# Performance work log

Measured on AMD Instinct MI355X. Metric: run time of the kernel, lower is better.

## Reference

```python
import jax, jax.numpy as jnp
import numpy as np

FEATS, HID, LAT = 128, 64, 16
T = 131072


def _prelu(x, a):
    return jnp.where(x > 0, x, a * x)


def setup_inputs() -> dict:
    key = jax.random.key(0)
    ks = jax.random.split(key, 24)
    s = 0.05
    inp = {
        "x": jax.random.normal(ks[0], (T, FEATS), jnp.float32),
        "eps": jax.random.normal(ks[1], (T, LAT), jnp.float32),
        "h0": jax.random.uniform(ks[2], (HID,), jnp.float32),
        "c0": jax.random.normal(ks[3], (HID,), jnp.float32),
        "training": 1,
        # LSTM (torch gate order i,f,g,o)
        "W_ih": jax.random.normal(ks[4], (4 * HID, FEATS), jnp.float32) * s,
        "W_hh": jax.random.normal(ks[5], (4 * HID, HID), jnp.float32) * s,
        "b_ih": jax.random.normal(ks[6], (4 * HID,), jnp.float32) * s,
        "b_hh": jax.random.normal(ks[7], (4 * HID,), jnp.float32) * s,
        # encoder: Linear(H,H) PReLU Linear(H,H) PReLU Linear(H,2L)
        "We1": jax.random.normal(ks[8], (HID, HID), jnp.float32) * s,
        "be1": jax.random.normal(ks[9], (HID,), jnp.float32) * s,
        "ae1": jnp.array(0.25, jnp.float32),
        "We2": jax.random.normal(ks[10], (HID, HID), jnp.float32) * s,
        "be2": jax.random.normal(ks[11], (HID,), jnp.float32) * s,
        "ae2": jnp.array(0.25, jnp.float32),
        "We3": jax.random.normal(ks[12], (2 * LAT, HID), jnp.float32) * s,
        "be3": jax.random.normal(ks[13], (2 * LAT,), jnp.float32) * s,
        # decoder: Linear(L,H) PReLU Linear(H,H) PReLU Linear(H,F) Tanh
        "Wd1": jax.random.normal(ks[14], (HID, LAT), jnp.float32) * s,
        "bd1": jax.random.normal(ks[15], (HID,), jnp.float32) * s,
        "ad1": jnp.array(0.25, jnp.float32),
        "Wd2": jax.random.normal(ks[16], (HID, HID), jnp.float32) * s,
        "bd2": jax.random.normal(ks[17], (HID,), jnp.float32) * s,
        "ad2": jnp.array(0.25, jnp.float32),
        "Wd3": jax.random.normal(ks[18], (FEATS, HID), jnp.float32) * s,
        "bd3": jax.random.normal(ks[19], (FEATS,), jnp.float32) * s,
    }
    return inp


def reference(x, eps, h0, c0, training, W_ih, W_hh, b_ih, b_hh,
              We1, be1, ae1, We2, be2, ae2, We3, be3,
              Wd1, bd1, ad1, Wd2, bd2, ad2, Wd3, bd3):
    b = b_ih + b_hh

    def step(carry, xs):
        h, c = carry
        xt, et = xs
        gates = xt @ W_ih.T + h @ W_hh.T + b          # [4H]
        i, f, g, o = jnp.split(gates, 4)
        i, f, o = jax.nn.sigmoid(i), jax.nn.sigmoid(f), jax.nn.sigmoid(o)
        c2 = f * c + i * jnp.tanh(g)
        h2 = o * jnp.tanh(c2)
        e = _prelu(h2 @ We1.T + be1, ae1)
        e = _prelu(e @ We2.T + be2, ae2)
        ml = e @ We3.T + be3                          # [2L]
        mu, lv = ml[:LAT], ml[LAT:]
        z = mu + et * jnp.exp(0.5 * lv) if training else mu
        d = _prelu(z @ Wd1.T + bd1, ad1)
        d = _prelu(d @ Wd2.T + bd2, ad2)
        out = 4.0 * jnp.tanh(d @ Wd3.T + bd3)         # [F]
        return (h2, c2), (out, mu, lv)

    (_, _), (outs, mus, lvs) = jax.lax.scan(step, (h0, c0), (x, eps))
    return outs, mus, lvs
```

## Files before the change

### kernel.cpp

```cpp
#include <hip/hip_runtime.h>
#include <cstdint>

#define T_STEPS 131072
#define FEATS 128
#define HID 64
#define LAT 16
#define GATES 256

typedef float v4f __attribute__((ext_vector_type(4)));

#define LOG2E 1.44269504088896340736f

__device__ __forceinline__ float frcp(float x) { return __builtin_amdgcn_rcpf(x); }
__device__ __forceinline__ float fexp2(float x) { return __builtin_amdgcn_exp2f(x); }

__device__ __forceinline__ float tanh_f(float x) {
  float ax = fabsf(x);
  float e = fexp2(ax * (-2.0f * LOG2E));
  float r = (1.0f - e) * frcp(1.0f + e);
  return copysignf(r, x);
}
__device__ __forceinline__ float prelu(float x, float a) { return x > 0.0f ? x : a * x; }

__global__ __launch_bounds__(256) void kA(const float* __restrict__ x,
                                          const float* __restrict__ W_ih,
                                          const float* __restrict__ b_ih,
                                          const float* __restrict__ b_hh,
                                          float* __restrict__ xg,
                                          int t0, int n) {
  __shared__ float wt[FEATS * 128];
  __shared__ __align__(16) float xb[4][FEATS];
  const int tid = threadIdx.x;
  const int w = tid >> 6, l = tid & 63;
  const int half = blockIdx.x & 1;
  const int pair = blockIdx.x >> 1;

  for (int idx = tid; idx < 128 * FEATS; idx += 256) {
    int jj = idx >> 7, k = idx & 127;
    wt[k * 128 + jj] = W_ih[(size_t)(half * 128 + jj) * FEATS + k];
  }
  const int j0 = half * 128 + 2 * l;
  const float b0 = b_ih[j0] + b_hh[j0];
  const float b1 = b_ih[j0 + 1] + b_hh[j0 + 1];
  __syncthreads();

  for (int s = pair * 4 + w; s < n; s += 1024) {
    const size_t t = (size_t)(t0 + s);
    *(float2*)&xb[w][2 * l] = *(const float2*)&x[t * FEATS + 2 * l];
    float a0 = b0, a0b = 0.f, a1 = b1, a1b = 0.f;
#pragma unroll
    for (int k = 0; k < FEATS; k += 4) {
      float4 xk = *(const float4*)&xb[w][k];
      float2 w0 = *(const float2*)&wt[(k + 0) * 128 + 2 * l];
      float2 w1 = *(const float2*)&wt[(k + 1) * 128 + 2 * l];
      float2 w2 = *(const float2*)&wt[(k + 2) * 128 + 2 * l];
      float2 w3 = *(const float2*)&wt[(k + 3) * 128 + 2 * l];
      a0  += xk.x * w0.x; a0b += xk.y * w1.x;
      a0  += xk.z * w2.x; a0b += xk.w * w3.x;
      a1  += xk.x * w0.y; a1b += xk.y * w1.y;
      a1  += xk.z * w2.y; a1b += xk.w * w3.y;
    }
    *(float2*)&xg[(size_t)s * GATES + j0] = make_float2(a0 + a0b, a1 + a1b);
  }
}

#define BAR() asm volatile("s_waitcnt lgkmcnt(0)\ns_barrier" ::: "memory")

__global__ __launch_bounds__(256, 1) void kB(const float* __restrict__ xg,
                                             const float* __restrict__ W_hh,
                                             const float* __restrict__ h0,
                                             const float* __restrict__ c0,
                                             float* __restrict__ state,
                                             float* __restrict__ h2out,
                                             int t0, int nsteps, int first) {
  __shared__ __align__(16) float hbuf[2][HID];
  const int tid = threadIdx.x;
  const int w = tid >> 6;
  const int lane = tid & 63;
  const int le = lane & 15;
  const int g = lane >> 4;
  const int e = (w << 4) | le;
  const int j = (g << 6) | e;
  const bool isg2 = (g == 2);
  const float kmul2 = isg2 ? (-2.0f * LOG2E) : (-LOG2E);
  const int adr_f = (16 + le) << 2;
  const int adr_g = (32 + le) << 2;
  const int adr_o = (48 + le) << 2;

  v4f wreg[16];
#pragma unroll
  for (int k = 0; k < 16; ++k) wreg[k] = *(const v4f*)&W_hh[(size_t)j * HID + 4 * k];

  if (tid < HID) hbuf[0][tid] = first ? h0[tid] : state[tid];
  float c_reg = (lane < 16) ? (first ? c0[e] : state[HID + e]) : 0.0f;

  float x0 = xg[(size_t)0 * GATES + j];
  float x1 = xg[(size_t)1 * GATES + j];
  float x2 = xg[(size_t)2 * GATES + j];
  float x3 = xg[(size_t)3 * GATES + j];
  __syncthreads();

#define LSTM_STEP(XV, S, CUR)                                              \
  {                                                                        \
    const v4f* hb4 = (const v4f*)hbuf[CUR];                                \
    v4f ac0 = {(XV), 0.f, 0.f, 0.f};                                       \
    v4f ac1 = {0.f, 0.f, 0.f, 0.f};                                        \
    v4f ac2 = {0.f, 0.f, 0.f, 0.f};                                        \
    v4f ac3 = {0.f, 0.f, 0.f, 0.f};                                        \
    _Pragma("unroll")                                                      \
    for (int kk = 0; kk < 16; kk += 4) {                                   \
      ac0 = __builtin_elementwise_fma(hb4[kk + 0], wreg[kk + 0], ac0);     \
      ac1 = __builtin_elementwise_fma(hb4[kk + 1], wreg[kk + 1], ac1);     \
      ac2 = __builtin_elementwise_fma(hb4[kk + 2], wreg[kk + 2], ac2);     \
      ac3 = __builtin_elementwise_fma(hb4[kk + 3], wreg[kk + 3], ac3);     \
    }                                                                      \
    v4f av = (ac0 + ac1) + (ac2 + ac3);                                    \
    float acc = (av.x + av.y) + (av.z + av.w);                             \
    float ax = fabsf(acc);                                                 \
    float e_ = fexp2(kmul2 * ax);                                          \
    float rn = frcp(1.0f + e_);                                            \
    float pos = isg2 ? (1.0f - e_) * rn : rn;                              \
    float neg = isg2 ? -pos : e_ * rn;                                     \
    float a = (acc >= 0.0f) ? pos : neg;                                   \
    int ai = __float_as_int(a);                                            \
    float fv = __int_as_float(__builtin_amdgcn_ds_bpermute(adr_f, ai));    \
    float gv = __int_as_float(__builtin_amdgcn_ds_bpermute(adr_g, ai));    \
    float ov = __int_as_float(__builtin_amdgcn_ds_bpermute(adr_o, ai));    \
    float c2 = fv * c_reg + a * gv;                                        \
    float h2v = ov * tanh_f(c2);                                           \
    c_reg = c2;                                                            \
    if (lane < 16) {                                                       \
      hbuf[(CUR) ^ 1][e] = h2v;                                            \
      h2out[(size_t)(t0 + (S)) * 128 + e] = h2v;                           \
    }                                                                      \
    BAR();                                                                 \
  }

  for (int s = 0; s < nsteps; s += 4) {
    { float nx = xg[(size_t)(s + 4) * GATES + j]; LSTM_STEP(x0, s + 0, 0); x0 = nx; }
    { float nx = xg[(size_t)(s + 5) * GATES + j]; LSTM_STEP(x1, s + 1, 1); x1 = nx; }
    { float nx = xg[(size_t)(s + 6) * GATES + j]; LSTM_STEP(x2, s + 2, 0); x2 = nx; }
    { float nx = xg[(size_t)(s + 7) * GATES + j]; LSTM_STEP(x3, s + 3, 1); x3 = nx; }
  }
  if (tid < HID) state[tid] = hbuf[0][tid];
  if (lane < 16) state[HID + e] = c_reg;
#undef LSTM_STEP
}

__device__ __forceinline__ void stageT(float* dst, const float* __restrict__ src,
                                       int rows, int colsShift, int tid, int nthr) {
  const int total = rows << colsShift;
  const int cmask = (1 << colsShift) - 1;
  for (int idx = tid; idx < total; idx += nthr) {
    int jr = idx >> colsShift, k = idx & cmask;
    dst[k * rows + jr] = src[idx];
  }
}

__global__ __launch_bounds__(512) void kC(const float* __restrict__ eps,
                                          const int* __restrict__ trainp,
                                          const float* __restrict__ We1, const float* __restrict__ be1, const float* __restrict__ ae1,
                                          const float* __restrict__ We2, const float* __restrict__ be2, const float* __restrict__ ae2,
                                          const float* __restrict__ We3, const float* __restrict__ be3,
                                          const float* __restrict__ Wd1, const float* __restrict__ bd1, const float* __restrict__ ad1,
                                          const float* __restrict__ Wd2, const float* __restrict__ bd2, const float* __restrict__ ad2,
                                          const float* __restrict__ Wd3, const float* __restrict__ bd3,
                                          float* __restrict__ out) {
  __shared__ float wt1[4096], wt2[4096], wt3[2048], wtd1[1024], wtd2[4096], wtd3[8192];
  __shared__ float bb[416];
  __shared__ __align__(16) float abuf[8][2][HID];
  const int tid = threadIdx.x;

  stageT(wt1, We1, 64, 6, tid, 512);
  stageT(wt2, We2, 64, 6, tid, 512);
  stageT(wt3, We3, 32, 6, tid, 512);
  stageT(wtd1, Wd1, 64, 4, tid, 512);
  stageT(wtd2, Wd2, 64, 6, tid, 512);
  stageT(wtd3, Wd3, 128, 6, tid, 512);
  for (int i = tid; i < 416; i += 512) {
    float v;
    if (i < 64)       v = be1[i];
    else if (i < 128) v = be2[i - 64];
    else if (i < 160) v = be3[i - 128];
    else if (i < 224) v = bd1[i - 160];
    else if (i < 288) v = bd2[i - 224];
    else              v = bd3[i - 288];
    bb[i] = v;
  }
  const float a1 = *ae1, a2 = *ae2, ad1v = *ad1, ad2v = *ad2;
  const int train = *trainp;
  __syncthreads();

  const int w = tid >> 6, l = tid & 63, le = l & 15;
  float* bufA = abuf[w][0];
  float* bufB = abuf[w][1];

  for (int it = 0; it < 64; ++it) {
    const size_t t = ((size_t)blockIdx.x << 9) + (size_t)(it << 3) + (size_t)w;
    bufA[l] = out[t * 128 + l];
    {
      float accA = bb[l], accB = 0.f;
#pragma unroll
      for (int k = 0; k < 64; k += 4) {
        float4 v = *(const float4*)&bufA[k];
        accA += v.x * wt1[(k + 0) * 64 + l];
        accB += v.y * wt1[(k + 1) * 64 + l];
        accA += v.z * wt1[(k + 2) * 64 + l];
        accB += v.w * wt1[(k + 3) * 64 + l];
      }
      bufB[l] = prelu(accA + accB, a1);
    }
    {
      float accA = bb[64 + l], accB = 0.f;
#pragma unroll
      for (int k = 0; k < 64; k += 4) {
        float4 v = *(const float4*)&bufB[k];
        accA += v.x * wt2[(k + 0) * 64 + l];
        accB += v.y * wt2[(k + 1) * 64 + l];
        accA += v.z * wt2[(k + 2) * 64 + l];
        accB += v.w * wt2[(k + 3) * 64 + l];
      }
      bufA[l] = prelu(accA + accB, a2);
    }
    float m;
    {
      const int jj = l & 31;
      float accA = bb[128 + jj], accB = 0.f;
#pragma unroll
      for (int k = 0; k < 64; k += 4) {
        float4 v = *(const float4*)&bufA[k];
        accA += v.x * wt3[(k + 0) * 32 + jj];
        accB += v.y * wt3[(k + 1) * 32 + jj];
        accA += v.z * wt3[(k + 2) * 32 + jj];
        accB += v.w * wt3[(k + 3) * 32 + jj];
      }
      m = accA + accB;
    }
    if (l < 16)      out[(size_t)T_STEPS * 128 + t * LAT + l] = m;
    else if (l < 32) out[(size_t)T_STEPS * 144 + t * LAT + (l - 16)] = m;
    float muv = __shfl(m, le);
    float lvv = __shfl(m, 16 + le);
    float ev = eps[t * LAT + le];
    float z = train ? (muv + ev * fexp2(0.5f * LOG2E * lvv)) : muv;
    if (l < 16) bufB[l] = z;
    {
      float accA = bb[160 + l], accB = 0.f;
#pragma unroll
      for (int k = 0; k < 16; k += 4) {
        float4 v = *(const float4*)&bufB[k];
        accA += v.x * wtd1[(k + 0) * 64 + l];
        accB += v.y * wtd1[(k + 1) * 64 + l];
        accA += v.z * wtd1[(k + 2) * 64 + l];
        accB += v.w * wtd1[(k + 3) * 64 + l];
      }
      bufA[l] = prelu(accA + accB, ad1v);
    }
    {
      float accA = bb[224 + l], accB = 0.f;
#pragma unroll
      for (int k = 0; k < 64; k += 4) {
        float4 v = *(const float4*)&bufA[k];
        accA += v.x * wtd2[(k + 0) * 64 + l];
        accB += v.y * wtd2[(k + 1) * 64 + l];
        accA += v.z * wtd2[(k + 2) * 64 + l];
        accB += v.w * wtd2[(k + 3) * 64 + l];
      }
      bufB[l] = prelu(accA + accB, ad2v);
    }
    {
      float acc0 = bb[288 + 2 * l], acc0b = 0.f;
      float acc1 = bb[288 + 2 * l + 1], acc1b = 0.f;
#pragma unroll
      for (int k = 0; k < 64; k += 2) {
        float2 v = *(const float2*)&bufB[k];
        float2 w0 = *(const float2*)&wtd3[(k + 0) * 128 + 2 * l];
        float2 w1 = *(const float2*)&wtd3[(k + 1) * 128 + 2 * l];
        acc0  += v.x * w0.x; acc0b += v.y * w1.x;
        acc1  += v.x * w0.y; acc1b += v.y * w1.y;
      }
      float o0 = 4.0f * tanh_f(acc0 + acc0b);
      float o1 = 4.0f * tanh_f(acc1 + acc1b);
      *(float2*)&out[t * 128 + 2 * l] = make_float2(o0, o1);
    }
  }
}

extern "C" void kernel_launch(void* const* d_in, const int* in_sizes, int n_in,
                              void* d_out, int out_size, void* d_ws, size_t ws_size,
                              hipStream_t stream) {
  (void)in_sizes; (void)n_in; (void)out_size;
  const float* x    = (const float*)d_in[0];
  const float* eps  = (const float*)d_in[1];
  const float* h0   = (const float*)d_in[2];
  const float* c0   = (const float*)d_in[3];
  const int*   tr   = (const int*)d_in[4];
  const float* W_ih = (const float*)d_in[5];
  const float* W_hh = (const float*)d_in[6];
  const float* b_ih = (const float*)d_in[7];
  const float* b_hh = (const float*)d_in[8];
  const float* We1  = (const float*)d_in[9];
  const float* be1  = (const float*)d_in[10];
  const float* ae1  = (const float*)d_in[11];
  const float* We2  = (const float*)d_in[12];
  const float* be2  = (const float*)d_in[13];
  const float* ae2  = (const float*)d_in[14];
  const float* We3  = (const float*)d_in[15];
  const float* be3  = (const float*)d_in[16];
  const float* Wd1  = (const float*)d_in[17];
  const float* bd1  = (const float*)d_in[18];
  const float* ad1  = (const float*)d_in[19];
  const float* Wd2  = (const float*)d_in[20];
  const float* bd2  = (const float*)d_in[21];
  const float* ad2  = (const float*)d_in[22];
  const float* Wd3  = (const float*)d_in[23];
  const float* bd3  = (const float*)d_in[24];
  float* out = (float*)d_out;

  char* ws = (char*)d_ws;
  float* state = (float*)ws;
  float* xg    = (float*)(ws + 1024);

  long fit = (ws_size > 2048) ? (long)((ws_size - 1024) / (GATES * sizeof(float))) - 8 : 0;
  long ch = (fit < (long)T_STEPS) ? fit : (long)T_STEPS;
  ch &= ~3L;
  if (ch < 1024) ch = 1024;

  for (long t0 = 0; t0 < T_STEPS; t0 += ch) {
    int n = (int)(((long)T_STEPS - t0 < ch) ? ((long)T_STEPS - t0) : ch);
    hipLaunchKernelGGL(kA, dim3(512), dim3(256), 0, stream,
                       x, W_ih, b_ih, b_hh, xg, (int)t0, n);
    hipLaunchKernelGGL(kB, dim3(1), dim3(256), 0, stream,
                       xg, W_hh, h0, c0, state, out, (int)t0, n, (t0 == 0) ? 1 : 0);
  }
  hipLaunchKernelGGL(kC, dim3(256), dim3(512), 0, stream,
                     eps, tr, We1, be1, ae1, We2, be2, ae2, We3, be3,
                     Wd1, bd1, ad1, Wd2, bd2, ad2, Wd3, bd3, out);
}
```

Measured before the change: 55.03 ms.

## Run LSTM recurrence in a single wavefront with per-unit gate ownership

Result: slower. 131.4 ms (+138.7%).

```diff
diff --git a/kernel.cpp b/kernel.cpp
--- a/kernel.cpp
+++ b/kernel.cpp
@@ -14,9 +14,13 @@
 __device__ __forceinline__ float frcp(float x) { return __builtin_amdgcn_rcpf(x); }
 __device__ __forceinline__ float fexp2(float x) { return __builtin_amdgcn_exp2f(x); }
 
+__device__ __forceinline__ float sigm_f(float x) {
+  float e = fexp2(-LOG2E * fabsf(x));
+  float r = frcp(1.0f + e);
+  return x >= 0.0f ? r : e * r;
+}
 __device__ __forceinline__ float tanh_f(float x) {
-  float ax = fabsf(x);
-  float e = fexp2(ax * (-2.0f * LOG2E));
+  float e = fexp2(-2.0f * LOG2E * fabsf(x));
   float r = (1.0f - e) * frcp(1.0f + e);
   return copysignf(r, x);
 }
@@ -42,6 +46,8 @@
   const int j0 = half * 128 + 2 * l;
   const float b0 = b_ih[j0] + b_hh[j0];
   const float b1 = b_ih[j0 + 1] + b_hh[j0 + 1];
+  const int g0 = j0 >> 6;
+  const int e0 = j0 & 63;
   __syncthreads();
 
   for (int s = pair * 4 + w; s < n; s += 1024) {
@@ -60,90 +66,79 @@
       a1  += xk.x * w0.y; a1b += xk.y * w1.y;
       a1  += xk.z * w2.y; a1b += xk.w * w3.y;
     }
-    *(float2*)&xg[(size_t)s * GATES + j0] = make_float2(a0 + a0b, a1 + a1b);
-  }
-}
-
-#define BAR() asm volatile("s_waitcnt lgkmcnt(0)\ns_barrier" ::: "memory")
-
-__global__ __launch_bounds__(256, 1) void kB(const float* __restrict__ xg,
-                                             const float* __restrict__ W_hh,
-                                             const float* __restrict__ h0,
-                                             const float* __restrict__ c0,
-                                             float* __restrict__ state,
-                                             float* __restrict__ h2out,
-                                             int t0, int nsteps, int first) {
-  __shared__ __align__(16) float hbuf[2][HID];
-  const int tid = threadIdx.x;
-  const int w = tid >> 6;
-  const int lane = tid & 63;
-  const int le = lane & 15;
-  const int g = lane >> 4;
-  const int e = (w << 4) | le;
-  const int j = (g << 6) | e;
-  const bool isg2 = (g == 2);
-  const float kmul2 = isg2 ? (-2.0f * LOG2E) : (-LOG2E);
-  const int adr_f = (16 + le) << 2;
-  const int adr_g = (32 + le) << 2;
-  const int adr_o = (48 + le) << 2;
-
-  v4f wreg[16];
-#pragma unroll
-  for (int k = 0; k < 16; ++k) wreg[k] = *(const v4f*)&W_hh[(size_t)j * HID + 4 * k];
-
-  if (tid < HID) hbuf[0][tid] = first ? h0[tid] : state[tid];
-  float c_reg = (lane < 16) ? (first ? c0[e] : state[HID + e]) : 0.0f;
-
-  float x0 = xg[(size_t)0 * GATES + j];
-  float x1 = xg[(size_t)1 * GATES + j];
-  float x2 = xg[(size_t)2 * GATES + j];
-  float x3 = xg[(size_t)3 * GATES + j];
-  __syncthreads();
-
-#define LSTM_STEP(XV, S, CUR)                                              \
+    float* dst = &xg[(size_t)s * GATES];
+    dst[e0 * 4 + g0]       = a0 + a0b;
+    dst[(e0 + 1) * 4 + g0] = a1 + a1b;
+  }
+}
+
+__global__ __launch_bounds__(64, 1) void kB(const float4* __restrict__ xg4,
+                                            const float* __restrict__ W_hh,
+                                            const float* __restrict__ h0,
+                                            const float* __restrict__ c0,
+                                            float* __restrict__ state,
+                                            float* __restrict__ h2out,
+                                            int t0, int nsteps, int first) {
+  __shared__ __align__(16) float hbuf[HID];
+  const int e = threadIdx.x;
+
+  v4f wi[16], wf[16], wg[16], wo[16];
+#pragma unroll
+  for (int k = 0; k < 16; ++k) {
+    wi[k] = *(const v4f*)&W_hh[(size_t)(0 * HID + e) * HID + 4 * k];
+    wf[k] = *(const v4f*)&W_hh[(size_t)(1 * HID + e) * HID + 4 * k];
+    wg[k] = *(const v4f*)&W_hh[(size_t)(2 * HID + e) * HID + 4 * k];
+    wo[k] = *(const v4f*)&W_hh[(size_t)(3 * HID + e) * HID + 4 * k];
+  }
+
+  hbuf[e] = first ? h0[e] : state[e];
+  float c_reg = first ? c0[e] : state[HID + e];
+  float hlast = 0.0f;
+
+  float4 x0 = xg4[(size_t)0 * HID + e];
+  float4 x1 = xg4[(size_t)1 * HID + e];
+  float4 x2 = xg4[(size_t)2 * HID + e];
+  float4 x3 = xg4[(size_t)3 * HID + e];
+
+#define LSTM_STEP(XV, S)                                                   \
   {                                                                        \
-    const v4f* hb4 = (const v4f*)hbuf[CUR];                                \
-    v4f ac0 = {(XV), 0.f, 0.f, 0.f};                                       \
-    v4f ac1 = {0.f, 0.f, 0.f, 0.f};                                        \
-    v4f ac2 = {0.f, 0.f, 0.f, 0.f};                                        \
-    v4f ac3 = {0.f, 0.f, 0.f, 0.f};                                        \
+    const v4f* hb = (const v4f*)hbuf;                                      \
+    v4f ai = {(XV).x, 0.f, 0.f, 0.f};                                      \
+    v4f af = {(XV).y, 0.f, 0.f, 0.f};                                      \
+    v4f ag = {(XV).z, 0.f, 0.f, 0.f};                                      \
+    v4f ao = {(XV).w, 0.f, 0.f, 0.f};                                      \
     _Pragma("unroll")                                                      \
-    for (int kk = 0; kk < 16; kk += 4) {                                   \
-      ac0 = __builtin_elementwise_fma(hb4[kk + 0], wreg[kk + 0], ac0);     \
-      ac1 = __builtin_elementwise_fma(hb4[kk + 1], wreg[kk + 1], ac1);     \
-      ac2 = __builtin_elementwise_fma(hb4[kk + 2], wreg[kk + 2], ac2);     \
-      ac3 = __builtin_elementwise_fma(hb4[kk + 3], wreg[kk + 3], ac3);     \
+    for (int kk = 0; kk < 16; ++kk) {                                      \
+      v4f h4 = hb[kk];                                                     \
+      ai = __builtin_elementwise_fma(h4, wi[kk], ai);                      \
+      af = __builtin_elementwise_fma(h4, wf[kk], af);                      \
+      ag = __builtin_elementwise_fma(h4, wg[kk], ag);                      \
+      ao = __builtin_elementwise_fma(h4, wo[kk], ao);                      \
     }                                                                      \
-    v4f av = (ac0 + ac1) + (ac2 + ac3);                                    \
-    float acc = (av.x + av.y) + (av.z + av.w);                             \
-    float ax = fabsf(acc);                                                 \
-    float e_ = fexp2(kmul2 * ax);                                          \
-    float rn = frcp(1.0f + e_);                                            \
-    float pos = isg2 ? (1.0f - e_) * rn : rn;                              \
-    float neg = isg2 ? -pos : e_ * rn;                                     \
-    float a = (acc >= 0.0f) ? pos : neg;                                   \
-    int ai = __float_as_int(a);                                            \
-    float fv = __int_as_float(__builtin_amdgcn_ds_bpermute(adr_f, ai));    \
-    float gv = __int_as_float(__builtin_amdgcn_ds_bpermute(adr_g, ai));    \
-    float ov = __int_as_float(__builtin_amdgcn_ds_bpermute(adr_o, ai));    \
-    float c2 = fv * c_reg + a * gv;                                        \
+    float gi = (ai.x + ai.y) + (ai.z + ai.w);                              \
+    float gf = (af.x + af.y) + (af.z + af.w);                              \
+    float gg = (ag.x + ag.y) + (ag.z + ag.w);                              \
+    float go = (ao.x + ao.y) + (ao.z + ao.w);                              \
+    float iv = sigm_f(gi);                                                 \
+    float fv = sigm_f(gf);                                                 \
+    float ov = sigm_f(go);                                                 \
+    float tg = tanh_f(gg);                                                 \
+    float c2 = fv * c_reg + iv * tg;                                       \
     float h2v = ov * tanh_f(c2);                                           \
     c_reg = c2;                                                            \
-    if (lane < 16) {                                                       \
-      hbuf[(CUR) ^ 1][e] = h2v;                                            \
-      h2out[(size_t)(t0 + (S)) * 128 + e] = h2v;                           \
-    }                                                                      \
-    BAR();                                                                 \
+    hlast = h2v;                                                           \
+    hbuf[e] = h2v;                                                         \
+    h2out[(size_t)(t0 + (S)) * 128 + e] = h2v;                             \
   }
 
   for (int s = 0; s < nsteps; s += 4) {
-    { float nx = xg[(size_t)(s + 4) * GATES + j]; LSTM_STEP(x0, s + 0, 0); x0 = nx; }
-    { float nx = xg[(size_t)(s + 5) * GATES + j]; LSTM_STEP(x1, s + 1, 1); x1 = nx; }
-    { float nx = xg[(size_t)(s + 6) * GATES + j]; LSTM_STEP(x2, s + 2, 0); x2 = nx; }
-    { float nx = xg[(size_t)(s + 7) * GATES + j]; LSTM_STEP(x3, s + 3, 1); x3 = nx; }
-  }
-  if (tid < HID) state[tid] = hbuf[0][tid];
-  if (lane < 16) state[HID + e] = c_reg;
+    { float4 nx = xg4[(size_t)(s + 4) * HID + e]; LSTM_STEP(x0, s + 0); x0 = nx; }
+    { float4 nx = xg4[(size_t)(s + 5) * HID + e]; LSTM_STEP(x1, s + 1); x1 = nx; }
+    { float4 nx = xg4[(size_t)(s + 6) * HID + e]; LSTM_STEP(x2, s + 2); x2 = nx; }
+    { float4 nx = xg4[(size_t)(s + 7) * HID + e]; LSTM_STEP(x3, s + 3); x3 = nx; }
+  }
+  state[e] = hlast;
+  state[HID + e] = c_reg;
 #undef LSTM_STEP
 }
 
@@ -329,8 +324,9 @@
     int n = (int)(((long)T_STEPS - t0 < ch) ? ((long)T_STEPS - t0) : ch);
     hipLaunchKernelGGL(kA, dim3(512), dim3(256), 0, stream,
                        x, W_ih, b_ih, b_hh, xg, (int)t0, n);
-    hipLaunchKernelGGL(kB, dim3(1), dim3(256), 0, stream,
-                       xg, W_hh, h0, c0, state, out, (int)t0, n, (t0 == 0) ? 1 : 0);
+    hipLaunchKernelGGL(kB, dim3(1), dim3(64), 0, stream,
+                       (const float4*)xg, W_hh, h0, c0, state, out, (int)t0, n,
+                       (t0 == 0) ? 1 : 0);
   }
   hipLaunchKernelGGL(kC, dim3(256), dim3(512), 0, stream,
                      eps, tr, We1, be1, ae1, We2, be2, ae2, We3, be3,
```
